# Kernel tuning notes

Hardware: AMD Instinct MI355X
Metric: run time of the kernel (lower is better)

Reference implementation:

```python
import jax, jax.numpy as jnp
import numpy as np

N = 50000      # nodes
E = 800000     # edges
F_IN = 16      # feature_size
D = 96         # d_model
G = 64         # graphs per batch


def _gcn_conv(x, W, b, src, dst, dis, num_nodes):
    # PyG GCNConv: out = D^{-1/2}(A+I)D^{-1/2} X W + b (self-loops already in src/dst)
    h = x @ W                                   # [N, out]
    norm = (dis[src] * dis[dst])[:, None]       # [E+N, 1]
    msg = h[src] * norm                         # gather + scale
    agg = jax.ops.segment_sum(msg, dst, num_segments=num_nodes)
    return agg + b


def _forward(x, W_init, b_init, W1, b1, W2, b2, W3, b3, W4, b4,
             Wo1, bo1, Wo2, bo2, edge_index, batch_index):
    act = jax.nn.leaky_relu  # default negative_slope=0.01, matches nn.LeakyReLU()
    n = x.shape[0]
    # add self-loops once; degree includes self-loop (PyG gcn_norm default)
    loop = jnp.arange(n, dtype=edge_index.dtype)
    src = jnp.concatenate([edge_index[0], loop])
    dst = jnp.concatenate([edge_index[1], loop])
    deg = jax.ops.segment_sum(jnp.ones_like(src, dtype=x.dtype), dst, num_segments=n)
    dis = jax.lax.rsqrt(deg)  # deg >= 1 due to self-loops

    h = act(_gcn_conv(x, W_init, b_init, src, dst, dis, n))
    h = act(_gcn_conv(h, W1, b1, src, dst, dis, n))
    h = act(_gcn_conv(h, W2, b2, src, dst, dis, n))
    h = act(_gcn_conv(h, W3, b3, src, dst, dis, n))
    h = act(_gcn_conv(h, W4, b4, src, dst, dis, n))

    # global max + mean pooling per graph
    gmax = jax.ops.segment_max(h, batch_index, num_segments=G)
    gsum = jax.ops.segment_sum(h, batch_index, num_segments=G)
    cnt = jax.ops.segment_sum(jnp.ones((n,), dtype=h.dtype), batch_index, num_segments=G)
    gmean = gsum / jnp.maximum(cnt, 1.0)[:, None]
    pooled = jnp.concatenate([gmax, gmean], axis=1)  # [G, 2D]

    out = act(pooled @ Wo1 + bo1)  # dropout is identity in eval
    out = out @ Wo2 + bo2          # [G, 1]
    return out


def setup_inputs() -> dict:
    key = jax.random.key(0)
    ks = jax.random.split(key, 16)
    def glorot(k, shape):
        lim = float(np.sqrt(6.0 / (shape[0] + shape[1])))
        return jax.random.uniform(k, shape, jnp.float32, -lim, lim)
    inp = {
        'x': jax.random.normal(ks[0], (N, F_IN), jnp.float32),
        'edge_index': jax.random.randint(ks[1], (2, E), 0, N, dtype=jnp.int64),
        'batch_index': jnp.sort(jax.random.randint(ks[2], (N,), 0, G, dtype=jnp.int64)),
        'W_init': glorot(ks[3], (F_IN, D)), 'b_init': jnp.zeros((D,), jnp.float32),
        'W1': glorot(ks[4], (D, D)), 'b1': jnp.zeros((D,), jnp.float32),
        'W2': glorot(ks[5], (D, D)), 'b2': jnp.zeros((D,), jnp.float32),
        'W3': glorot(ks[6], (D, D)), 'b3': jnp.zeros((D,), jnp.float32),
        'W4': glorot(ks[7], (D, D)), 'b4': jnp.zeros((D,), jnp.float32),
        'Wo1': glorot(ks[8], (2 * D, D)), 'bo1': jnp.zeros((D,), jnp.float32),
        'Wo2': glorot(ks[9], (D, 1)), 'bo2': jnp.zeros((1,), jnp.float32),
    }
    return inp


def reference(x, edge_index, batch_index, W_init, b_init, W1, b1, W2, b2,
              W3, b3, W4, b4, Wo1, bo1, Wo2, bo2):
    return _forward(x, W_init, b_init, W1, b1, W2, b2, W3, b3, W4, b4,
                    Wo1, bo1, Wo2, bo2, edge_index, batch_index)
```

## Files before the change

kernel.cpp:

```cpp
#include <hip/hip_runtime.h>
#include <hip/hip_fp16.h>
#include <math.h>

#define LEAKY(x) ((x) > 0.f ? (x) : 0.01f * (x))
#define BK_SHIFT 9
#define NBMAX 128
#define BCAP 16384

typedef _Float16 half8 __attribute__((ext_vector_type(8)));
typedef float f32x4 __attribute__((ext_vector_type(4)));

__device__ __forceinline__ void add4(float4& acc, const float4& v) {
    acc.x += v.x; acc.y += v.y; acc.z += v.z; acc.w += v.w;
}

__global__ __launch_bounds__(256) void bin_kernel(const int* __restrict__ src,
                                                  const int* __restrict__ dst,
                                                  int* __restrict__ bfill,
                                                  uint2* __restrict__ tmp,
                                                  int E, int nb) {
    __shared__ int hist[NBMAX];
    __shared__ int scanbuf[NBMAX];
    __shared__ int lofs[NBMAX];
    __shared__ int adj[NBMAX];
    __shared__ uint2 buf[2048];
    __shared__ unsigned char bkt_of[2048];
    int base = blockIdx.x * 2048;
    int cnt = min(2048, E - base);
    int tid = threadIdx.x;
    for (int b = tid; b < NBMAX; b += 256) hist[b] = 0;
    __syncthreads();
    int es[8], ed[8];
#pragma unroll
    for (int k = 0; k < 8; ++k) {
        int l = tid + k * 256;
        if (l < cnt) {
            es[k] = src[base + l];
            ed[k] = dst[base + l];
            atomicAdd(&hist[ed[k] >> BK_SHIFT], 1);
        }
    }
    __syncthreads();
    if (tid < NBMAX) scanbuf[tid] = hist[tid];
    __syncthreads();
    for (int off = 1; off < NBMAX; off <<= 1) {
        int t = (tid < NBMAX && tid >= off) ? scanbuf[tid - off] : 0;
        __syncthreads();
        if (tid < NBMAX) scanbuf[tid] += t;
        __syncthreads();
    }
    if (tid < nb) {
        int cb = hist[tid];
        int start = scanbuf[tid] - cb;
        lofs[tid] = start;
        int g = (cb > 0) ? atomicAdd(&bfill[tid], cb) : 0;
        adj[tid] = tid * BCAP + g - start;
    }
    __syncthreads();
#pragma unroll
    for (int k = 0; k < 8; ++k) {
        int l = tid + k * 256;
        if (l < cnt) {
            int b = ed[k] >> BK_SHIFT;
            int r = atomicAdd(&lofs[b], 1);
            buf[r] = make_uint2((unsigned)es[k], (unsigned)ed[k]);
            bkt_of[r] = (unsigned char)b;
        }
    }
    __syncthreads();
    for (int j = tid; j < cnt; j += 256) {
        int b = bkt_of[j];
        tmp[adj[b] + j] = buf[j];
    }
}

__global__ __launch_bounds__(512) void place2(const uint2* __restrict__ tmp,
                                              const int* __restrict__ bfill,
                                              const float* __restrict__ X,
                                              float* __restrict__ dis,
                                              int* __restrict__ row_ptr,
                                              int* __restrict__ edge_src,
                                              float* __restrict__ Z0, int kq,
                                              int n, int E, int nb) {
    __shared__ int hist[512];
    __shared__ int sc[512];
    __shared__ int sbf[NBMAX];
    __shared__ int bb_s;
    int b = blockIdx.x;
    int tid = threadIdx.x;
    if (tid < NBMAX) sbf[tid] = (tid < nb) ? bfill[tid] : 0;
    hist[tid] = 0;
    __syncthreads();
    if (tid == 0) {
        int s = 0;
        for (int k = 0; k < b; ++k) s += sbf[k];
        bb_s = s;
    }
    __syncthreads();
    int bb = bb_s;
    int cnt = sbf[b];
    const uint2* mybkt = tmp + (size_t)b * BCAP;
    int node0 = b << BK_SHIFT;
    for (int j = tid; j < cnt; j += 512)
        atomicAdd(&hist[(int)mybkt[j].y - node0], 1);
    __syncthreads();
    int v = hist[tid];
    sc[tid] = v;
    __syncthreads();
    for (int off = 1; off < 512; off <<= 1) {
        int t = (tid >= off) ? sc[tid - off] : 0;
        __syncthreads();
        sc[tid] += t;
        __syncthreads();
    }
    int excl = sc[tid] - v;
    int i = node0 + tid;
    if (i < n) {
        row_ptr[i] = bb + excl;
        float di = rsqrtf((float)(v + 1));
        dis[i] = di;
        const float4* X4 = (const float4*)X;
        float4* Z4 = (float4*)Z0;
        for (int j = 0; j < kq; ++j) {
            float4 xv = X4[(size_t)i * kq + j];
            Z4[(size_t)i * kq + j] = make_float4(di * xv.x, di * xv.y, di * xv.z, di * xv.w);
        }
    }
    if (b == 0 && tid == 0) row_ptr[n] = E;
    __syncthreads();
    hist[tid] = bb + excl;
    __syncthreads();
    for (int j = tid; j < cnt; j += 512) {
        uint2 ev = mybkt[j];
        int pos = atomicAdd(&hist[(int)ev.y - node0], 1);
        edge_src[pos] = (int)ev.x;
    }
}

template <int LPN, int F4PL, int UNROLL>
__global__ __launch_bounds__(256) void agg_wave(const float* __restrict__ Z,
                                                const float* __restrict__ dis,
                                                const int* __restrict__ row_ptr,
                                                const int* __restrict__ edge_src,
                                                float* __restrict__ A, int n) {
    constexpr int GROUPS = 64 / LPN;
    constexpr int KQ = LPN * F4PL;
    int i = (blockIdx.x * 256 + threadIdx.x) >> 6;
    if (i >= n) return;
    int lane = threadIdx.x & 63;
    int g = lane / LPN;
    int c = lane % LPN;
    const float4* Z4 = (const float4*)Z;
    float di = dis[i];
    size_t base = (size_t)i * KQ + c * F4PL;
    float4 acc[F4PL];
    if (g == 0) {
#pragma unroll
        for (int j = 0; j < F4PL; ++j) acc[j] = Z4[base + j];
    } else {
#pragma unroll
        for (int j = 0; j < F4PL; ++j) acc[j] = make_float4(0.f, 0.f, 0.f, 0.f);
    }
    int re0 = row_ptr[i], re1 = row_ptr[i + 1];
#pragma unroll UNROLL
    for (int e = re0 + g; e < re1; e += GROUPS) {
        int s = edge_src[e];
        size_t sb = (size_t)s * KQ + c * F4PL;
#pragma unroll
        for (int j = 0; j < F4PL; ++j) {
            float4 xs = Z4[sb + j];
            add4(acc[j], xs);
        }
    }
#pragma unroll
    for (int m = LPN; m < 64; m <<= 1) {
#pragma unroll
        for (int j = 0; j < F4PL; ++j) {
            acc[j].x += __shfl_xor(acc[j].x, m);
            acc[j].y += __shfl_xor(acc[j].y, m);
            acc[j].z += __shfl_xor(acc[j].z, m);
            acc[j].w += __shfl_xor(acc[j].w, m);
        }
    }
    if (g == 0) {
#pragma unroll
        for (int j = 0; j < F4PL; ++j) {
            float4 o = make_float4(di * acc[j].x, di * acc[j].y,
                                   di * acc[j].z, di * acc[j].w);
            ((float4*)A)[base + j] = o;
        }
    }
}

__global__ __launch_bounds__(256) void agg_wave_h(const __half* __restrict__ Zh,
                                                  const float* __restrict__ dis,
                                                  const int* __restrict__ row_ptr,
                                                  const int* __restrict__ edge_src,
                                                  float* __restrict__ A, int n) {
    int i = (blockIdx.x * 256 + threadIdx.x) >> 6;
    if (i >= n) return;
    int lane = threadIdx.x & 63;
    int g = lane >> 3;
    int c = lane & 7;
    float di = dis[i];
    float acc[12];
    if (g == 0) {
        const uint2* zp = (const uint2*)(Zh + (size_t)i * 96 + c * 12);
#pragma unroll
        for (int k = 0; k < 3; ++k) {
            uint2 u = zp[k];
            float2 f0 = __half22float2(*(const __half2*)&u.x);
            float2 f1 = __half22float2(*(const __half2*)&u.y);
            acc[k * 4 + 0] = f0.x; acc[k * 4 + 1] = f0.y;
            acc[k * 4 + 2] = f1.x; acc[k * 4 + 3] = f1.y;
        }
    } else {
#pragma unroll
        for (int k = 0; k < 12; ++k) acc[k] = 0.f;
    }
    int re0 = row_ptr[i], re1 = row_ptr[i + 1];
#pragma unroll 4
    for (int e = re0 + g; e < re1; e += 8) {
        int s = edge_src[e];
        const uint2* zp = (const uint2*)(Zh + (size_t)s * 96 + c * 12);
        uint2 u0 = zp[0], u1 = zp[1], u2 = zp[2];
        float2 f;
        f = __half22float2(*(const __half2*)&u0.x); acc[0] += f.x; acc[1] += f.y;
        f = __half22float2(*(const __half2*)&u0.y); acc[2] += f.x; acc[3] += f.y;
        f = __half22float2(*(const __half2*)&u1.x); acc[4] += f.x; acc[5] += f.y;
        f = __half22float2(*(const __half2*)&u1.y); acc[6] += f.x; acc[7] += f.y;
        f = __half22float2(*(const __half2*)&u2.x); acc[8] += f.x; acc[9] += f.y;
        f = __half22float2(*(const __half2*)&u2.y); acc[10] += f.x; acc[11] += f.y;
    }
#pragma unroll
    for (int m = 8; m < 64; m <<= 1) {
#pragma unroll
        for (int k = 0; k < 12; ++k) acc[k] += __shfl_xor(acc[k], m);
    }
    if (g == 0) {
        float4* ap = (float4*)(A + (size_t)i * 96 + c * 12);
#pragma unroll
        for (int k = 0; k < 3; ++k)
            ap[k] = make_float4(di * acc[k * 4 + 0], di * acc[k * 4 + 1],
                                di * acc[k * 4 + 2], di * acc[k * 4 + 3]);
    }
}

template <bool SCALE, bool OUTH>
__global__ __launch_bounds__(256) void gemm_mfma(const float* __restrict__ A,
                                                 const float* __restrict__ W,
                                                 const float* __restrict__ b,
                                                 const float* __restrict__ dis,
                                                 void* __restrict__ Xn, int n) {
    constexpr int LDA = 104;
    __shared__ __align__(16) _Float16 Ah[64 * LDA];
    __shared__ __align__(16) _Float16 Wt[96 * LDA];
    int tid = threadIdx.x;
    int i0 = blockIdx.x * 64;
    for (int idx = tid; idx < 64 * 24; idx += 256) {
        int r = idx / 24, c4 = idx % 24;
        int gi = i0 + r;
        float4 v = (gi < n) ? ((const float4*)A)[(size_t)gi * 24 + c4]
                            : make_float4(0.f, 0.f, 0.f, 0.f);
        _Float16* p = &Ah[r * LDA + c4 * 4];
        p[0] = (_Float16)v.x; p[1] = (_Float16)v.y;
        p[2] = (_Float16)v.z; p[3] = (_Float16)v.w;
    }
    for (int idx = tid; idx < 96 * 24; idx += 256) {
        int k = idx / 24, c4 = idx % 24;
        float4 v = ((const float4*)W)[(size_t)k * 24 + c4];
        int nc = c4 * 4;
        Wt[(nc + 0) * LDA + k] = (_Float16)v.x;
        Wt[(nc + 1) * LDA + k] = (_Float16)v.y;
        Wt[(nc + 2) * LDA + k] = (_Float16)v.z;
        Wt[(nc + 3) * LDA + k] = (_Float16)v.w;
    }
    __syncthreads();
    int w = tid >> 6, lane = tid & 63;
    int q = lane >> 4, c = lane & 15;
    half8 af[3];
#pragma unroll
    for (int kc = 0; kc < 3; ++kc)
        af[kc] = *(const half8*)&Ah[(w * 16 + c) * LDA + kc * 32 + q * 8];
    float dvals[4];
#pragma unroll
    for (int r = 0; r < 4; ++r) {
        int gi = i0 + w * 16 + q * 4 + r;
        dvals[r] = (SCALE && gi < n) ? dis[gi] : 1.f;
    }
#pragma unroll
    for (int nt = 0; nt < 6; ++nt) {
        f32x4 acc = {0.f, 0.f, 0.f, 0.f};
#pragma unroll
        for (int kc = 0; kc < 3; ++kc) {
            half8 bf = *(const half8*)&Wt[(nt * 16 + c) * LDA + kc * 32 + q * 8];
            acc = __builtin_amdgcn_mfma_f32_16x16x32_f16(af[kc], bf, acc, 0, 0, 0);
        }
        int col = nt * 16 + c;
        float bias = b[col];
#pragma unroll
        for (int r = 0; r < 4; ++r) {
            int gi = i0 + w * 16 + q * 4 + r;
            if (gi < n) {
                float v = acc[r] + bias;
                v = LEAKY(v);
                if (SCALE) v *= dvals[r];
                if (OUTH)
                    ((_Float16*)Xn)[(size_t)gi * 96 + col] = (_Float16)v;
                else
                    ((float*)Xn)[(size_t)gi * 96 + col] = v;
            }
        }
    }
}

__global__ __launch_bounds__(192) void gemm_l0(const float* __restrict__ A,
                                               const float* __restrict__ W,
                                               const float* __restrict__ b,
                                               const float* __restrict__ dis,
                                               __half* __restrict__ Xn, int n) {
    constexpr int KQ = 4;
    __shared__ __align__(16) float4 Al[64 * KQ];
    int tid = threadIdx.x;
    int i0 = blockIdx.x * 64;
    for (int idx = tid; idx < 64 * KQ; idx += 192) {
        int gi = i0 + idx / KQ;
        Al[idx] = (gi < n) ? ((const float4*)A)[(size_t)i0 * KQ + idx]
                           : make_float4(0.f, 0.f, 0.f, 0.f);
    }
    __syncthreads();
    int fq = tid % 24;
    int g = tid / 24;
    const float4* W4 = (const float4*)W;
    float4 bb = ((const float4*)b)[fq];
    float4 acc[8];
#pragma unroll
    for (int r = 0; r < 8; ++r) acc[r] = bb;
    for (int kc = 0; kc < 16; kc += 8) {
        float4 w[8];
#pragma unroll
        for (int kk = 0; kk < 8; ++kk) w[kk] = W4[(size_t)(kc + kk) * 24 + fq];
#pragma unroll
        for (int r = 0; r < 8; ++r) {
            const float4* ar = &Al[(g * 8 + r) * KQ + (kc >> 2)];
#pragma unroll
            for (int k4 = 0; k4 < 2; ++k4) {
                float4 a = ar[k4];
                float4 w0 = w[4 * k4 + 0], w1 = w[4 * k4 + 1];
                float4 w2 = w[4 * k4 + 2], w3 = w[4 * k4 + 3];
                acc[r].x += a.x * w0.x + a.y * w1.x + a.z * w2.x + a.w * w3.x;
                acc[r].y += a.x * w0.y + a.y * w1.y + a.z * w2.y + a.w * w3.y;
                acc[r].z += a.x * w0.z + a.y * w1.z + a.z * w2.z + a.w * w3.z;
                acc[r].w += a.x * w0.w + a.y * w1.w + a.z * w2.w + a.w * w3.w;
            }
        }
    }
#pragma unroll
    for (int r = 0; r < 8; ++r) {
        int gi = i0 + g * 8 + r;
        if (gi < n) {
            float di = dis[gi];
            float4 o;
            o.x = di * LEAKY(acc[r].x); o.y = di * LEAKY(acc[r].y);
            o.z = di * LEAKY(acc[r].z); o.w = di * LEAKY(acc[r].w);
            __half2 h0 = __floats2half2_rn(o.x, o.y);
            __half2 h1 = __floats2half2_rn(o.z, o.w);
            uint2 u;
            u.x = *(unsigned*)&h0;
            u.y = *(unsigned*)&h1;
            ((uint2*)Xn)[(size_t)gi * 24 + fq] = u;
        }
    }
}

__device__ __forceinline__ int lower_bound(const int* b, int n, int v) {
    int lo = 0, hi = n;
    while (lo < hi) {
        int m = (lo + hi) >> 1;
        if (b[m] < v) lo = m + 1; else hi = m;
    }
    return lo;
}

__global__ void pool_partial(const float* __restrict__ X, const int* __restrict__ batch,
                             float* __restrict__ pmax, float* __restrict__ psum, int n) {
    int g = blockIdx.x / 8, ch = blockIdx.x % 8;
    int f = threadIdx.x;
    int s = lower_bound(batch, n, g), e = lower_bound(batch, n, g + 1);
    int len = e - s;
    int cs = s + (int)((long)len * ch / 8);
    int ce = s + (int)((long)len * (ch + 1) / 8);
    float mx = -INFINITY, sm = 0.f;
    for (int i = cs; i < ce; ++i) {
        float v = X[(size_t)i * 96 + f];
        mx = fmaxf(mx, v);
        sm += v;
    }
    pmax[(size_t)blockIdx.x * 96 + f] = mx;
    psum[(size_t)blockIdx.x * 96 + f] = sm;
}

__global__ void pool_final(const float* __restrict__ pmax, const float* __restrict__ psum,
                           const int* __restrict__ batch,
                           const float* __restrict__ Wo1, const float* __restrict__ bo1,
                           const float* __restrict__ Wo2, const float* __restrict__ bo2,
                           float* __restrict__ out, int n) {
    __shared__ float pooled[192];
    __shared__ float sh[96];
    int g = blockIdx.x, f = threadIdx.x;
    float mx = -INFINITY, sm = 0.f;
    for (int c = 0; c < 8; ++c) {
        mx = fmaxf(mx, pmax[(size_t)(g * 8 + c) * 96 + f]);
        sm += psum[(size_t)(g * 8 + c) * 96 + f];
    }
    int s = lower_bound(batch, n, g), e = lower_bound(batch, n, g + 1);
    float cnt = fmaxf((float)(e - s), 1.f);
    pooled[f] = mx;
    pooled[96 + f] = sm / cnt;
    __syncthreads();
    float acc = bo1[f];
    for (int k = 0; k < 192; ++k) acc += pooled[k] * Wo1[k * 96 + f];
    float a = LEAKY(acc);
    sh[f] = a * Wo2[f];
    __syncthreads();
    if (f == 0) {
        float sacc = 0.f;
        for (int k = 0; k < 96; ++k) sacc += sh[k];
        out[g] = sacc + bo2[0];
    }
}

extern "C" void kernel_launch(void* const* d_in, const int* in_sizes, int n_in,
                              void* d_out, int out_size, void* d_ws, size_t ws_size,
                              hipStream_t stream) {
    const float* x      = (const float*)d_in[0];
    const int*   eidx   = (const int*)d_in[1];
    const int*   batch  = (const int*)d_in[2];
    const float* W_init = (const float*)d_in[3];
    const float* b_init = (const float*)d_in[4];
    const float* W1 = (const float*)d_in[5];  const float* b1 = (const float*)d_in[6];
    const float* W2 = (const float*)d_in[7];  const float* b2 = (const float*)d_in[8];
    const float* W3 = (const float*)d_in[9];  const float* b3 = (const float*)d_in[10];
    const float* W4 = (const float*)d_in[11]; const float* b4 = (const float*)d_in[12];
    const float* Wo1 = (const float*)d_in[13]; const float* bo1 = (const float*)d_in[14];
    const float* Wo2 = (const float*)d_in[15]; const float* bo2 = (const float*)d_in[16];
    float* out = (float*)d_out;

    const int N = in_sizes[2];
    const int E = in_sizes[1] / 2;
    const int G = out_size;
    const int* src = eidx;
    const int* dst = eidx + E;

    char* ws = (char*)d_ws;
    size_t off = 0;
    auto alloc = [&](size_t bytes) {
        size_t o = off;
        off += (bytes + 255) & ~(size_t)255;
        return o;
    };
    float* dis       = (float*)(ws + alloc((size_t)N * 4));
    int*   row_ptr   = (int*)(ws + alloc((size_t)(N + 1) * 4));
    int*   bfill     = (int*)(ws + alloc(NBMAX * 4));
    int*   edge_src  = (int*)(ws + alloc((size_t)E * 4));
    float* Z0        = (float*)(ws + alloc((size_t)N * 16 * 4));
    __half* ZA       = (__half*)(ws + alloc((size_t)N * 96 * 2));
    __half* ZB       = (__half*)(ws + alloc((size_t)N * 96 * 2));
    float* H         = (float*)(ws + alloc((size_t)N * 96 * 4));
    float* Agg       = (float*)(ws + alloc((size_t)N * 96 * 4));
    float* pmax      = (float*)(ws + alloc((size_t)G * 8 * 96 * 4));
    float* psum      = (float*)(ws + alloc((size_t)G * 8 * 96 * 4));
    uint2* tmp       = (uint2*)Agg;
    (void)ws_size; (void)n_in;

    const int nbBkt  = (N + (1 << BK_SHIFT) - 1) >> BK_SHIFT;
    const int nbWave = (N + 3) / 4;
    const int nbTile = (N + 63) / 64;

    hipMemsetAsync(bfill, 0, NBMAX * 4, stream);
    bin_kernel<<<(E + 2047) / 2048, 256, 0, stream>>>(src, dst, bfill, tmp, E, nbBkt);
    place2<<<nbBkt, 512, 0, stream>>>(tmp, bfill, x, dis, row_ptr, edge_src, Z0,
                                      4, N, E, nbBkt);

    agg_wave<4, 1, 2><<<nbWave, 256, 0, stream>>>(Z0, dis, row_ptr, edge_src, Agg, N);
    gemm_l0<<<nbTile, 192, 0, stream>>>(Agg, W_init, b_init, dis, ZA, N);

    const float* Ws[4] = {W1, W2, W3, W4};
    const float* bs[4] = {b1, b2, b3, b4};
    __half* cur = ZA;
    __half* nxt = ZB;
    for (int l = 0; l < 4; ++l) {
        agg_wave_h<<<nbWave, 256, 0, stream>>>(cur, dis, row_ptr, edge_src, Agg, N);
        if (l < 3) {
            gemm_mfma<true, true><<<nbTile, 256, 0, stream>>>(Agg, Ws[l], bs[l],
                                                              dis, nxt, N);
            __half* t = cur; cur = nxt; nxt = t;
        } else {
            gemm_mfma<false, false><<<nbTile, 256, 0, stream>>>(Agg, Ws[l], bs[l],
                                                                dis, H, N);
        }
    }

    pool_partial<<<G * 8, 96, 0, stream>>>(H, batch, pmax, psum, N);
    pool_final<<<G, 96, 0, stream>>>(pmax, psum, batch, Wo1, bo1, Wo2, bo2, out, N);
}
```

Before: 378.9 us.

## Store fp16 aggregates, pre-transpose weights, fuse last GEMM with pooling

Aggregation now writes fp16 output and accumulates with v_fma_mix instructions, loading edge indices with nontemporal hints. GEMM kernels read fp16 A directly from global memory and use weights converted and transposed once by a prep kernel, so they no longer stage tiles through LDS. The final layer's GEMM does the max/sum pooling itself with atomics, which removes the fp32 H buffer and the pool_partial pass. The prep kernel also replaces the memset. In exchange this adds atomic contention and fp16 rounding of the aggregates.

```diff
diff --git a/kernel.cpp b/kernel.cpp
--- a/kernel.cpp
+++ b/kernel.cpp
@@ -12,6 +12,48 @@
 
 __device__ __forceinline__ void add4(float4& acc, const float4& v) {
     acc.x += v.x; acc.y += v.y; acc.z += v.z; acc.w += v.w;
+}
+
+#define FMIX_LO(acc, u, one) \
+    asm("v_fma_mix_f32 %0, %1, %2, %0 op_sel:[0,0,0] op_sel_hi:[1,0,0]" \
+        : "+v"(acc) : "v"(u), "v"(one))
+#define FMIX_HI(acc, u, one) \
+    asm("v_fma_mix_f32 %0, %1, %2, %0 op_sel:[1,0,0] op_sel_hi:[1,0,0]" \
+        : "+v"(acc) : "v"(u), "v"(one))
+
+__device__ __forceinline__ unsigned encf(float f) {
+    unsigned u = __float_as_uint(f);
+    return (u & 0x80000000u) ? ~u : (u | 0x80000000u);
+}
+__device__ __forceinline__ float decf(unsigned u) {
+    if (u == 0u) return -INFINITY;
+    unsigned b = (u & 0x80000000u) ? (u & 0x7fffffffu) : ~u;
+    return __uint_as_float(b);
+}
+
+__global__ __launch_bounds__(256) void prep(const float* __restrict__ W1,
+                                            const float* __restrict__ W2,
+                                            const float* __restrict__ W3,
+                                            const float* __restrict__ W4,
+                                            _Float16* __restrict__ WtG,
+                                            int* __restrict__ bfill,
+                                            unsigned* __restrict__ gmaxU,
+                                            float* __restrict__ gsum, int G) {
+    int bi = blockIdx.x, tid = threadIdx.x;
+    if (bi < 4) {
+        const float* W = bi == 0 ? W1 : bi == 1 ? W2 : bi == 2 ? W3 : W4;
+        _Float16* dst = WtG + bi * 9216;
+        for (int idx = tid; idx < 9216; idx += 256) {
+            int k = idx / 96, nn = idx % 96;
+            dst[nn * 96 + k] = (_Float16)W[idx];
+        }
+    } else if (bi == 4) {
+        for (int i2 = tid; i2 < NBMAX; i2 += 256) bfill[i2] = 0;
+    } else if (bi == 5) {
+        for (int i2 = tid; i2 < G * 96; i2 += 256) gmaxU[i2] = 0u;
+    } else {
+        for (int i2 = tid; i2 < G * 96; i2 += 256) gsum[i2] = 0.f;
+    }
 }
 
 __global__ __launch_bounds__(256) void bin_kernel(const int* __restrict__ src,
@@ -196,41 +238,39 @@
                                                   const float* __restrict__ dis,
                                                   const int* __restrict__ row_ptr,
                                                   const int* __restrict__ edge_src,
-                                                  float* __restrict__ A, int n) {
+                                                  __half* __restrict__ A, int n) {
     int i = (blockIdx.x * 256 + threadIdx.x) >> 6;
     if (i >= n) return;
     int lane = threadIdx.x & 63;
     int g = lane >> 3;
     int c = lane & 7;
     float di = dis[i];
+    float one = 1.0f;
     float acc[12];
+#pragma unroll
+    for (int k = 0; k < 12; ++k) acc[k] = 0.f;
     if (g == 0) {
         const uint2* zp = (const uint2*)(Zh + (size_t)i * 96 + c * 12);
-#pragma unroll
-        for (int k = 0; k < 3; ++k) {
-            uint2 u = zp[k];
-            float2 f0 = __half22float2(*(const __half2*)&u.x);
-            float2 f1 = __half22float2(*(const __half2*)&u.y);
-            acc[k * 4 + 0] = f0.x; acc[k * 4 + 1] = f0.y;
-            acc[k * 4 + 2] = f1.x; acc[k * 4 + 3] = f1.y;
-        }
-    } else {
-#pragma unroll
-        for (int k = 0; k < 12; ++k) acc[k] = 0.f;
+        uint2 u0 = zp[0], u1 = zp[1], u2 = zp[2];
+        FMIX_LO(acc[0], u0.x, one); FMIX_HI(acc[1], u0.x, one);
+        FMIX_LO(acc[2], u0.y, one); FMIX_HI(acc[3], u0.y, one);
+        FMIX_LO(acc[4], u1.x, one); FMIX_HI(acc[5], u1.x, one);
+        FMIX_LO(acc[6], u1.y, one); FMIX_HI(acc[7], u1.y, one);
+        FMIX_LO(acc[8], u2.x, one); FMIX_HI(acc[9], u2.x, one);
+        FMIX_LO(acc[10], u2.y, one); FMIX_HI(acc[11], u2.y, one);
     }
     int re0 = row_ptr[i], re1 = row_ptr[i + 1];
 #pragma unroll 4
     for (int e = re0 + g; e < re1; e += 8) {
-        int s = edge_src[e];
+        int s = __builtin_nontemporal_load(&edge_src[e]);
         const uint2* zp = (const uint2*)(Zh + (size_t)s * 96 + c * 12);
         uint2 u0 = zp[0], u1 = zp[1], u2 = zp[2];
-        float2 f;
-        f = __half22float2(*(const __half2*)&u0.x); acc[0] += f.x; acc[1] += f.y;
-        f = __half22float2(*(const __half2*)&u0.y); acc[2] += f.x; acc[3] += f.y;
-        f = __half22float2(*(const __half2*)&u1.x); acc[4] += f.x; acc[5] += f.y;
-        f = __half22float2(*(const __half2*)&u1.y); acc[6] += f.x; acc[7] += f.y;
-        f = __half22float2(*(const __half2*)&u2.x); acc[8] += f.x; acc[9] += f.y;
-        f = __half22float2(*(const __half2*)&u2.y); acc[10] += f.x; acc[11] += f.y;
+        FMIX_LO(acc[0], u0.x, one); FMIX_HI(acc[1], u0.x, one);
+        FMIX_LO(acc[2], u0.y, one); FMIX_HI(acc[3], u0.y, one);
+        FMIX_LO(acc[4], u1.x, one); FMIX_HI(acc[5], u1.x, one);
+        FMIX_LO(acc[6], u1.y, one); FMIX_HI(acc[7], u1.y, one);
+        FMIX_LO(acc[8], u2.x, one); FMIX_HI(acc[9], u2.x, one);
+        FMIX_LO(acc[10], u2.y, one); FMIX_HI(acc[11], u2.y, one);
     }
 #pragma unroll
     for (int m = 8; m < 64; m <<= 1) {
@@ -238,50 +278,44 @@
         for (int k = 0; k < 12; ++k) acc[k] += __shfl_xor(acc[k], m);
     }
     if (g == 0) {
-        float4* ap = (float4*)(A + (size_t)i * 96 + c * 12);
-#pragma unroll
-        for (int k = 0; k < 3; ++k)
-            ap[k] = make_float4(di * acc[k * 4 + 0], di * acc[k * 4 + 1],
-                                di * acc[k * 4 + 2], di * acc[k * 4 + 3]);
-    }
-}
-
-template <bool SCALE, bool OUTH>
-__global__ __launch_bounds__(256) void gemm_mfma(const float* __restrict__ A,
-                                                 const float* __restrict__ W,
+        __half2 h0 = __floats2half2_rn(di * acc[0], di * acc[1]);
+        __half2 h1 = __floats2half2_rn(di * acc[2], di * acc[3]);
+        __half2 h2 = __floats2half2_rn(di * acc[4], di * acc[5]);
+        __half2 h3 = __floats2half2_rn(di * acc[6], di * acc[7]);
+        __half2 h4 = __floats2half2_rn(di * acc[8], di * acc[9]);
+        __half2 h5 = __floats2half2_rn(di * acc[10], di * acc[11]);
+        uint2 o0, o1, o2;
+        o0.x = *(unsigned*)&h0; o0.y = *(unsigned*)&h1;
+        o1.x = *(unsigned*)&h2; o1.y = *(unsigned*)&h3;
+        o2.x = *(unsigned*)&h4; o2.y = *(unsigned*)&h5;
+        uint2* ap = (uint2*)(A + (size_t)i * 96 + c * 12);
+        ap[0] = o0; ap[1] = o1; ap[2] = o2;
+    }
+}
+
+template <bool SCALE>
+__global__ __launch_bounds__(256) void gemm_mfma(const __half* __restrict__ A,
+                                                 const _Float16* __restrict__ Wt,
                                                  const float* __restrict__ b,
                                                  const float* __restrict__ dis,
-                                                 void* __restrict__ Xn, int n) {
-    constexpr int LDA = 104;
-    __shared__ __align__(16) _Float16 Ah[64 * LDA];
-    __shared__ __align__(16) _Float16 Wt[96 * LDA];
+                                                 __half* __restrict__ Xn, int n) {
     int tid = threadIdx.x;
     int i0 = blockIdx.x * 64;
-    for (int idx = tid; idx < 64 * 24; idx += 256) {
-        int r = idx / 24, c4 = idx % 24;
-        int gi = i0 + r;
-        float4 v = (gi < n) ? ((const float4*)A)[(size_t)gi * 24 + c4]
-                            : make_float4(0.f, 0.f, 0.f, 0.f);
-        _Float16* p = &Ah[r * LDA + c4 * 4];
-        p[0] = (_Float16)v.x; p[1] = (_Float16)v.y;
-        p[2] = (_Float16)v.z; p[3] = (_Float16)v.w;
-    }
-    for (int idx = tid; idx < 96 * 24; idx += 256) {
-        int k = idx / 24, c4 = idx % 24;
-        float4 v = ((const float4*)W)[(size_t)k * 24 + c4];
-        int nc = c4 * 4;
-        Wt[(nc + 0) * LDA + k] = (_Float16)v.x;
-        Wt[(nc + 1) * LDA + k] = (_Float16)v.y;
-        Wt[(nc + 2) * LDA + k] = (_Float16)v.z;
-        Wt[(nc + 3) * LDA + k] = (_Float16)v.w;
-    }
-    __syncthreads();
     int w = tid >> 6, lane = tid & 63;
     int q = lane >> 4, c = lane & 15;
+    int arow = i0 + w * 16 + c;
+    const _Float16* Ap = (const _Float16*)A;
     half8 af[3];
-#pragma unroll
-    for (int kc = 0; kc < 3; ++kc)
-        af[kc] = *(const half8*)&Ah[(w * 16 + c) * LDA + kc * 32 + q * 8];
+    if (arow < n) {
+#pragma unroll
+        for (int kc = 0; kc < 3; ++kc)
+            af[kc] = *(const half8*)&Ap[(size_t)arow * 96 + kc * 32 + q * 8];
+    } else {
+#pragma unroll
+        for (int kc = 0; kc < 3; ++kc)
+#pragma unroll
+            for (int j = 0; j < 8; ++j) af[kc][j] = (_Float16)0.f;
+    }
     float dvals[4];
 #pragma unroll
     for (int r = 0; r < 4; ++r) {
@@ -293,7 +327,7 @@
         f32x4 acc = {0.f, 0.f, 0.f, 0.f};
 #pragma unroll
         for (int kc = 0; kc < 3; ++kc) {
-            half8 bf = *(const half8*)&Wt[(nt * 16 + c) * LDA + kc * 32 + q * 8];
+            half8 bf = *(const half8*)&Wt[(size_t)(nt * 16 + c) * 96 + kc * 32 + q * 8];
             acc = __builtin_amdgcn_mfma_f32_16x16x32_f16(af[kc], bf, acc, 0, 0, 0);
         }
         int col = nt * 16 + c;
@@ -305,12 +339,95 @@
                 float v = acc[r] + bias;
                 v = LEAKY(v);
                 if (SCALE) v *= dvals[r];
-                if (OUTH)
-                    ((_Float16*)Xn)[(size_t)gi * 96 + col] = (_Float16)v;
-                else
-                    ((float*)Xn)[(size_t)gi * 96 + col] = v;
+                ((_Float16*)Xn)[(size_t)gi * 96 + col] = (_Float16)v;
             }
         }
+    }
+}
+
+__global__ __launch_bounds__(256) void gemm_pool(const __half* __restrict__ A,
+                                                 const _Float16* __restrict__ Wt,
+                                                 const float* __restrict__ b,
+                                                 const int* __restrict__ batch,
+                                                 unsigned* __restrict__ gmaxU,
+                                                 float* __restrict__ gsum, int n) {
+    __shared__ float pmaxs[4][96];
+    __shared__ float psums[4][96];
+    int tid = threadIdx.x;
+    int i0 = blockIdx.x * 64;
+    int w = tid >> 6, lane = tid & 63;
+    int q = lane >> 4, c = lane & 15;
+    int arow = i0 + w * 16 + c;
+    const _Float16* Ap = (const _Float16*)A;
+    half8 af[3];
+    if (arow < n) {
+#pragma unroll
+        for (int kc = 0; kc < 3; ++kc)
+            af[kc] = *(const half8*)&Ap[(size_t)arow * 96 + kc * 32 + q * 8];
+    } else {
+#pragma unroll
+        for (int kc = 0; kc < 3; ++kc)
+#pragma unroll
+            for (int j = 0; j < 8; ++j) af[kc][j] = (_Float16)0.f;
+    }
+    int row0 = i0 + w * 16;
+    bool wuni = (row0 + 15 < n) && (batch[row0] == batch[row0 + 15]);
+    bool buni = (i0 + 63 < n) && (batch[i0] == batch[i0 + 63]);
+    int gw = wuni ? batch[row0] : 0;
+#pragma unroll
+    for (int nt = 0; nt < 6; ++nt) {
+        f32x4 acc = {0.f, 0.f, 0.f, 0.f};
+#pragma unroll
+        for (int kc = 0; kc < 3; ++kc) {
+            half8 bf = *(const half8*)&Wt[(size_t)(nt * 16 + c) * 96 + kc * 32 + q * 8];
+            acc = __builtin_amdgcn_mfma_f32_16x16x32_f16(af[kc], bf, acc, 0, 0, 0);
+        }
+        int col = nt * 16 + c;
+        float bias = b[col];
+        float v[4];
+#pragma unroll
+        for (int r = 0; r < 4; ++r) {
+            float t = acc[r] + bias;
+            v[r] = LEAKY(t);
+        }
+        if (wuni) {
+            float mx = fmaxf(fmaxf(v[0], v[1]), fmaxf(v[2], v[3]));
+            float sm = v[0] + v[1] + v[2] + v[3];
+            mx = fmaxf(mx, __shfl_xor(mx, 16)); sm += __shfl_xor(sm, 16);
+            mx = fmaxf(mx, __shfl_xor(mx, 32)); sm += __shfl_xor(sm, 32);
+            if (buni) {
+                if (q == 0) { pmaxs[w][col] = mx; psums[w][col] = sm; }
+            } else if (q == 0) {
+                atomicMax(&gmaxU[gw * 96 + col], encf(mx));
+                atomicAdd(&gsum[gw * 96 + col], sm);
+            }
+        } else {
+            int r = 0;
+            while (r < 4) {
+                int gi = i0 + w * 16 + q * 4 + r;
+                if (gi >= n) break;
+                int gb = batch[gi];
+                float mx = v[r], sm = v[r];
+                int r2 = r + 1;
+                for (; r2 < 4; ++r2) {
+                    int gi2 = i0 + w * 16 + q * 4 + r2;
+                    if (gi2 >= n || batch[gi2] != gb) break;
+                    mx = fmaxf(mx, v[r2]); sm += v[r2];
+                }
+                atomicMax(&gmaxU[gb * 96 + col], encf(mx));
+                atomicAdd(&gsum[gb * 96 + col], sm);
+                r = r2;
+            }
+        }
+    }
+    __syncthreads();
+    if (buni && tid < 96) {
+        float m = fmaxf(fmaxf(pmaxs[0][tid], pmaxs[1][tid]),
+                        fmaxf(pmaxs[2][tid], pmaxs[3][tid]));
+        float s = psums[0][tid] + psums[1][tid] + psums[2][tid] + psums[3][tid];
+        int gb = batch[i0];
+        atomicMax(&gmaxU[gb * 96 + tid], encf(m));
+        atomicAdd(&gsum[gb * 96 + tid], s);
     }
 }
 
@@ -382,25 +499,8 @@
     return lo;
 }
 
-__global__ void pool_partial(const float* __restrict__ X, const int* __restrict__ batch,
-                             float* __restrict__ pmax, float* __restrict__ psum, int n) {
-    int g = blockIdx.x / 8, ch = blockIdx.x % 8;
-    int f = threadIdx.x;
-    int s = lower_bound(batch, n, g), e = lower_bound(batch, n, g + 1);
-    int len = e - s;
-    int cs = s + (int)((long)len * ch / 8);
-    int ce = s + (int)((long)len * (ch + 1) / 8);
-    float mx = -INFINITY, sm = 0.f;
-    for (int i = cs; i < ce; ++i) {
-        float v = X[(size_t)i * 96 + f];
-        mx = fmaxf(mx, v);
-        sm += v;
-    }
-    pmax[(size_t)blockIdx.x * 96 + f] = mx;
-    psum[(size_t)blockIdx.x * 96 + f] = sm;
-}
-
-__global__ void pool_final(const float* __restrict__ pmax, const float* __restrict__ psum,
+__global__ void pool_final(const unsigned* __restrict__ gmaxU,
+                           const float* __restrict__ gsum,
                            const int* __restrict__ batch,
                            const float* __restrict__ Wo1, const float* __restrict__ bo1,
                            const float* __restrict__ Wo2, const float* __restrict__ bo2,
@@ -408,15 +508,10 @@
     __shared__ float pooled[192];
     __shared__ float sh[96];
     int g = blockIdx.x, f = threadIdx.x;
-    float mx = -INFINITY, sm = 0.f;
-    for (int c = 0; c < 8; ++c) {
-        mx = fmaxf(mx, pmax[(size_t)(g * 8 + c) * 96 + f]);
-        sm += psum[(size_t)(g * 8 + c) * 96 + f];
-    }
     int s = lower_bound(batch, n, g), e = lower_bound(batch, n, g + 1);
     float cnt = fmaxf((float)(e - s), 1.f);
-    pooled[f] = mx;
-    pooled[96 + f] = sm / cnt;
+    pooled[f] = decf(gmaxU[(size_t)g * 96 + f]);
+    pooled[96 + f] = gsum[(size_t)g * 96 + f] / cnt;
     __syncthreads();
     float acc = bo1[f];
     for (int k = 0; k < 192; ++k) acc += pooled[k] * Wo1[k * 96 + f];
@@ -452,6 +547,8 @@
     const int* src = eidx;
     const int* dst = eidx + E;
 
+    const int nbBkt  = (N + (1 << BK_SHIFT) - 1) >> BK_SHIFT;
+
     char* ws = (char*)d_ws;
     size_t off = 0;
     auto alloc = [&](size_t bytes) {
@@ -459,48 +556,46 @@
         off += (bytes + 255) & ~(size_t)255;
         return o;
     };
-    float* dis       = (float*)(ws + alloc((size_t)N * 4));
-    int*   row_ptr   = (int*)(ws + alloc((size_t)(N + 1) * 4));
-    int*   bfill     = (int*)(ws + alloc(NBMAX * 4));
-    int*   edge_src  = (int*)(ws + alloc((size_t)E * 4));
-    float* Z0        = (float*)(ws + alloc((size_t)N * 16 * 4));
-    __half* ZA       = (__half*)(ws + alloc((size_t)N * 96 * 2));
-    __half* ZB       = (__half*)(ws + alloc((size_t)N * 96 * 2));
-    float* H         = (float*)(ws + alloc((size_t)N * 96 * 4));
-    float* Agg       = (float*)(ws + alloc((size_t)N * 96 * 4));
-    float* pmax      = (float*)(ws + alloc((size_t)G * 8 * 96 * 4));
-    float* psum      = (float*)(ws + alloc((size_t)G * 8 * 96 * 4));
-    uint2* tmp       = (uint2*)Agg;
+    float*    dis      = (float*)(ws + alloc((size_t)N * 4));
+    int*      row_ptr  = (int*)(ws + alloc((size_t)(N + 1) * 4));
+    int*      bfill    = (int*)(ws + alloc(NBMAX * 4));
+    unsigned* gmaxU    = (unsigned*)(ws + alloc((size_t)G * 96 * 4));
+    float*    gsumB    = (float*)(ws + alloc((size_t)G * 96 * 4));
+    int*      edge_src = (int*)(ws + alloc((size_t)E * 4));
+    float*    Z0       = (float*)(ws + alloc((size_t)N * 16 * 4));
+    __half*   ZA       = (__half*)(ws + alloc((size_t)N * 96 * 2));
+    __half*   ZB       = (__half*)(ws + alloc((size_t)N * 96 * 2));
+    __half*   AggH     = (__half*)(ws + alloc((size_t)N * 96 * 2));
+    float*    Agg0     = (float*)(ws + alloc((size_t)N * 16 * 4));
+    _Float16* WtG      = (_Float16*)(ws + alloc((size_t)4 * 9216 * 2));
+    uint2*    tmp      = (uint2*)(ws + alloc((size_t)nbBkt * BCAP * 8));
     (void)ws_size; (void)n_in;
 
-    const int nbBkt  = (N + (1 << BK_SHIFT) - 1) >> BK_SHIFT;
     const int nbWave = (N + 3) / 4;
     const int nbTile = (N + 63) / 64;
 
-    hipMemsetAsync(bfill, 0, NBMAX * 4, stream);
+    prep<<<7, 256, 0, stream>>>(W1, W2, W3, W4, WtG, bfill, gmaxU, gsumB, G);
     bin_kernel<<<(E + 2047) / 2048, 256, 0, stream>>>(src, dst, bfill, tmp, E, nbBkt);
     place2<<<nbBkt, 512, 0, stream>>>(tmp, bfill, x, dis, row_ptr, edge_src, Z0,
                                       4, N, E, nbBkt);
 
-    agg_wave<4, 1, 2><<<nbWave, 256, 0, stream>>>(Z0, dis, row_ptr, edge_src, Agg, N);
-    gemm_l0<<<nbTile, 192, 0, stream>>>(Agg, W_init, b_init, dis, ZA, N);
-
-    const float* Ws[4] = {W1, W2, W3, W4};
+    agg_wave<4, 1, 2><<<nbWave, 256, 0, stream>>>(Z0, dis, row_ptr, edge_src, Agg0, N);
+    gemm_l0<<<nbTile, 192, 0, stream>>>(Agg0, W_init, b_init, dis, ZA, N);
+
     const float* bs[4] = {b1, b2, b3, b4};
     __half* cur = ZA;
     __half* nxt = ZB;
     for (int l = 0; l < 4; ++l) {
-        agg_wave_h<<<nbWave, 256, 0, stream>>>(cur, dis, row_ptr, edge_src, Agg, N);
+        agg_wave_h<<<nbWave, 256, 0, stream>>>(cur, dis, row_ptr, edge_src, AggH, N);
         if (l < 3) {
-            gemm_mfma<true, true><<<nbTile, 256, 0, stream>>>(Agg, Ws[l], bs[l],
-                                                              dis, nxt, N);
+            gemm_mfma<true><<<nbTile, 256, 0, stream>>>(AggH, WtG + l * 9216, bs[l],
+                                                        dis, nxt, N);
             __half* t = cur; cur = nxt; nxt = t;
         } else {
-            gemm_mfma<false, false><<<nbTile, 256, 0, stream>>>(Agg, Ws[l], bs[l],
-                                                                dis, H, N);
-        }
-    }
-
-    pool_partial<<<G * 8, 96, 0, stream>>>(H, batch, pmax, psum, N);
-    pool_final<<<G, 96, 0, stream>>>(pmax, psum, batch, Wo1, bo1, Wo2, bo2, out, N);
-}
+            gemm_pool<<<nbTile, 256, 0, stream>>>(AggH, WtG + 3 * 9216, bs[3],
+                                                  batch, gmaxU, gsumB, N);
+        }
+    }
+
+    pool_final<<<G, 96, 0, stream>>>(gmaxU, gsumB, batch, Wo1, bo1, Wo2, bo2, out, N);
+}
```

Measured after the change: 344.6 us. 1.1x faster.
